# Kernel optimization log

Measured on AMD Instinct MI355X. Metric: run time of the kernel, lower is better.

Reference implementation:

```python
import jax, jax.numpy as jnp
import numpy as np

DIM = 768
HEADS = 12
DIM_HEAD = 64
INNER = HEADS * DIM_HEAD  # 768
B, N = 8, 1024
SCALE = DIM_HEAD ** -0.5


def setup_inputs() -> dict:
    key = jax.random.key(0)
    ks = jax.random.split(key, 8)
    std = 0.02
    x = jax.random.normal(ks[0], (B, N, DIM), dtype=jnp.float32)
    W_q = jax.random.normal(ks[1], (DIM, INNER), dtype=jnp.float32) * std
    W_kv = jax.random.normal(ks[2], (DIM, 2 * INNER), dtype=jnp.float32) * std
    mix_pre = jax.random.normal(ks[3], (HEADS, HEADS), dtype=jnp.float32)
    mix_post = jax.random.normal(ks[4], (HEADS, HEADS), dtype=jnp.float32)
    W_out = jax.random.normal(ks[5], (INNER, DIM), dtype=jnp.float32) * std
    b_out = jnp.zeros((DIM,), dtype=jnp.float32)
    return {"x": x, "W_q": W_q, "W_kv": W_kv, "mix_pre": mix_pre,
            "mix_post": mix_post, "W_out": W_out, "b_out": b_out}


def reference(x, W_q, W_kv, mix_pre, mix_post, W_out, b_out):
    b, n, _ = x.shape
    # projections (context == x since no cross-attn context given)
    q = x @ W_q                                   # (b, n, inner)
    kv = x @ W_kv                                 # (b, n, 2*inner)
    k, v = jnp.split(kv, 2, axis=-1)
    # (b, n, h*d) -> (b, h, n, d)
    split_heads = lambda t: t.reshape(b, n, HEADS, DIM_HEAD).transpose(0, 2, 1, 3)
    q, k, v = split_heads(q), split_heads(k), split_heads(v)
    dots = jnp.einsum('bhid,bhjd->bhij', q, k) * SCALE
    dots = jnp.einsum('bhij,hg->bgij', dots, mix_pre)    # pre-softmax talking heads
    attn = jax.nn.softmax(dots, axis=-1)
    attn = jnp.einsum('bhij,hg->bgij', attn, mix_post)   # post-softmax talking heads
    out = jnp.einsum('bhij,bhjd->bhid', attn, v)         # (b, h, n, d)
    out = out.transpose(0, 2, 1, 3).reshape(b, n, INNER)
    return out @ W_out + b_out
```

## Files before the change

### kernel.cpp

```cpp
#include <hip/hip_runtime.h>
#include <hip/hip_bf16.h>

typedef __attribute__((ext_vector_type(8))) short short8_t;
typedef __attribute__((ext_vector_type(8))) unsigned short ushort8_t;
typedef __attribute__((ext_vector_type(4))) float f32x4;

#define SCALE 0.125f

__device__ __forceinline__ unsigned short f32_to_bf16_rne(float f) {
  unsigned int u = __float_as_uint(f);
  unsigned int r = 0x7FFFu + ((u >> 16) & 1u);
  return (unsigned short)((u + r) >> 16);
}

__device__ __forceinline__ int swz(int i) { return (i + (i >> 2)) & 3; }

__global__ __launch_bounds__(256) void cast_x_kernel(const float4* __restrict__ in,
                                                     ushort4* __restrict__ out, int n4) {
  int i = blockIdx.x * 256 + threadIdx.x;
  if (i < n4) {
    float4 v = in[i];
    ushort4 o;
    o.x = f32_to_bf16_rne(v.x); o.y = f32_to_bf16_rne(v.y);
    o.z = f32_to_bf16_rne(v.z); o.w = f32_to_bf16_rne(v.w);
    out[i] = o;
  }
}

__global__ __launch_bounds__(256) void transpose_cast_kernel(const float* __restrict__ in,
                                                             unsigned short* __restrict__ out,
                                                             int R, int C) {
  __shared__ float tile[32][33];
  int c0 = blockIdx.x * 32, r0 = blockIdx.y * 32;
  int tx = threadIdx.x & 31, ty = threadIdx.x >> 5;
  #pragma unroll
  for (int i = ty; i < 32; i += 8)
    tile[i][tx] = in[(long)(r0 + i) * C + c0 + tx];
  __syncthreads();
  #pragma unroll
  for (int i = ty; i < 32; i += 8)
    out[(long)(c0 + i) * R + r0 + tx] = f32_to_bf16_rne(tile[tx][i]);
}

__global__ __launch_bounds__(256) void transpose_v_kernel(const unsigned short* __restrict__ KV,
                                                          unsigned short* __restrict__ Vt) {
  __shared__ unsigned short tile[64][72];
  const int j0 = blockIdx.x * 64, h = blockIdx.y, b = blockIdx.z;
  const int tid = threadIdx.x;
  for (int c = tid; c < 512; c += 256) {
    int j = c >> 3, dp = (c & 7) * 8;
    *(ushort8_t*)&tile[j][dp] =
        *(const ushort8_t*)&KV[(long)(b * 1024 + j0 + j) * 1536 + 768 + h * 64 + dp];
  }
  __syncthreads();
  for (int c = tid; c < 512; c += 256) {
    int d = c >> 3, jp = (c & 7) * 8;
    ushort8_t v;
    #pragma unroll
    for (int t = 0; t < 8; t++) v[t] = tile[jp + t][d];
    int jg = j0 + jp;
    int jt_ = jg >> 5;
    int u = (jg >> 3) & 3;
    *(ushort8_t*)&Vt[((long)(b * 12 + h) * 64 + d) * 1024 + (jt_ << 5) + ((u ^ swz(d)) << 3)] = v;
  }
}

template <int BM, int BN, bool OUT_F32, bool BIAS, bool SUM2>
__global__ __launch_bounds__(256) void gemm_nt(const unsigned short* __restrict__ A,
                                               const unsigned short* __restrict__ A2, int lda,
                                               const unsigned short* __restrict__ B, int ldb,
                                               void* __restrict__ Cv, int ldc,
                                               const float* __restrict__ bias,
                                               int M, int N, int K) {
  constexpr int BK = 32;
  constexpr int LDT = BK + 8;
  __shared__ unsigned short As[BM][LDT];
  __shared__ unsigned short Bs[BN][LDT];
  const int m0 = blockIdx.y * BM;
  const int n0 = blockIdx.x * BN;
  const int tid = threadIdx.x;
  const int lane = tid & 63;
  const int w = tid >> 6;
  constexpr int WM = BM / 2, WN = BN / 2;
  constexpr int FM = WM / 16, FN = WN / 16;
  const int wr = w >> 1, wc = w & 1;

  f32x4 acc[FM][FN];
  #pragma unroll
  for (int a = 0; a < FM; a++)
    #pragma unroll
    for (int b2 = 0; b2 < FN; b2++) acc[a][b2] = (f32x4){0.f, 0.f, 0.f, 0.f};

  const int rl = lane & 15;
  const int kq = (lane >> 4) * 8;

  for (int k0 = 0; k0 < K; k0 += BK) {
    __syncthreads();
    for (int c = tid; c < BM * (BK / 8); c += 256) {
      int row = c >> 2, kp = (c & 3) * 8;
      ushort8_t v = *(const ushort8_t*)&A[(long)(m0 + row) * lda + k0 + kp];
      if (SUM2) {
        ushort8_t v2 = *(const ushort8_t*)&A2[(long)(m0 + row) * lda + k0 + kp];
        #pragma unroll
        for (int x = 0; x < 8; ++x)
          v[x] = f32_to_bf16_rne(__uint_as_float((unsigned)v[x] << 16) +
                                 __uint_as_float((unsigned)v2[x] << 16));
      }
      *(ushort8_t*)&As[row][kp] = v;
    }
    for (int c = tid; c < BN * (BK / 8); c += 256) {
      int row = c >> 2, kp = (c & 3) * 8;
      *(ushort8_t*)&Bs[row][kp] = *(const ushort8_t*)&B[(long)(n0 + row) * ldb + k0 + kp];
    }
    __syncthreads();
    short8_t af[FM], bfr[FN];
    #pragma unroll
    for (int fm = 0; fm < FM; fm++) af[fm] = *(const short8_t*)&As[wr * WM + fm * 16 + rl][kq];
    #pragma unroll
    for (int fn = 0; fn < FN; fn++) bfr[fn] = *(const short8_t*)&Bs[wc * WN + fn * 16 + rl][kq];
    #pragma unroll
    for (int fm = 0; fm < FM; fm++)
      #pragma unroll
      for (int fn = 0; fn < FN; fn++)
        acc[fm][fn] = __builtin_amdgcn_mfma_f32_16x16x32_bf16(af[fm], bfr[fn], acc[fm][fn], 0, 0, 0);
  }

  const int rq4 = (lane >> 4) * 4;
  #pragma unroll
  for (int fm = 0; fm < FM; fm++)
    #pragma unroll
    for (int fn = 0; fn < FN; fn++)
      #pragma unroll
      for (int j = 0; j < 4; j++) {
        int row = m0 + wr * WM + fm * 16 + rq4 + j;
        int col = n0 + wc * WN + fn * 16 + rl;
        float v = acc[fm][fn][j];
        if (BIAS) v += bias[col];
        if (OUT_F32)
          ((float*)Cv)[(long)row * ldc + col] = v;
        else
          ((unsigned short*)Cv)[(long)row * ldc + col] = f32_to_bf16_rne(v);
      }
}

__global__ __launch_bounds__(256, 2) void qk_mix_exp_kernel(
    const unsigned short* __restrict__ Qb, const unsigned short* __restrict__ KVb,
    const float* __restrict__ mix_pre,
    unsigned short* __restrict__ Eo, float* __restrict__ Lpart, int b_base) {
  __shared__ unsigned short Kbuf[24576];
  __shared__ unsigned short Qdb[8192];
  __shared__ float mpre_s[144];
  const int jt = blockIdx.x, it = blockIdx.y, z = blockIdx.z;
  const int b = b_base + z;
  const int tid = threadIdx.x, lane = tid & 63, w = tid >> 6;
  const int r15 = lane & 15, q = lane >> 4;
  if (tid < 144) mpre_s[tid] = mix_pre[tid] * SCALE;
  const int i0 = it * 64, j0 = jt * 32;

  ushort8_t kreg[12];
  #pragma unroll
  for (int u = 0; u < 12; ++u) {
    int unit = u * 256 + tid;
    int j = unit / 96, s = unit - j * 96;
    kreg[u] = *(const ushort8_t*)&KVb[(long)(b * 1024 + j0 + j) * 1536 + ((s ^ (j & 7)) << 3)];
  }
  ushort8_t qreg[2];
  #pragma unroll
  for (int u = 0; u < 2; ++u) {
    int unit = u * 256 + tid;
    int i = unit >> 3, s = unit & 7;
    qreg[u] = *(const ushort8_t*)&Qb[(long)(b * 1024 + i0 + i) * 768 + ((s ^ (i & 7)) << 3)];
  }
  #pragma unroll
  for (int u = 0; u < 12; ++u) *(ushort8_t*)&Kbuf[(u * 256 + tid) * 8] = kreg[u];
  #pragma unroll
  for (int u = 0; u < 2; ++u) *(ushort8_t*)&Qdb[(u * 256 + tid) * 8] = qreg[u];
  __syncthreads();

  float macc[12][2][4];
  #pragma unroll
  for (int g = 0; g < 12; ++g)
    #pragma unroll
    for (int nf = 0; nf < 2; ++nf)
      #pragma unroll
      for (int e = 0; e < 4; ++e) macc[g][nf][e] = 0.f;

  const int ar = w * 16 + r15, ax = ar & 7;

  for (int h = 0; h < 12; ++h) {
    if (h < 11) {
      #pragma unroll
      for (int u = 0; u < 2; ++u) {
        int unit = u * 256 + tid;
        int i = unit >> 3, s = unit & 7;
        qreg[u] = *(const ushort8_t*)&Qb[(long)(b * 1024 + i0 + i) * 768 + (h + 1) * 64 +
                                         ((s ^ (i & 7)) << 3)];
      }
    }
    const unsigned short* Qcur = &Qdb[(h & 1) * 4096];
    short8_t a0 = *(const short8_t*)&Qcur[ar * 64 + ((q ^ ax) << 3)];
    short8_t a1 = *(const short8_t*)&Qcur[ar * 64 + (((4 + q) ^ ax) << 3)];
    f32x4 h0 = {0.f, 0.f, 0.f, 0.f}, h1 = {0.f, 0.f, 0.f, 0.f};
    {
      const int br = r15, bx = br & 7;
      short8_t b0 = *(const short8_t*)&Kbuf[br * 768 + (((h * 8 + q) ^ bx) << 3)];
      short8_t b1 = *(const short8_t*)&Kbuf[br * 768 + (((h * 8 + 4 + q) ^ bx) << 3)];
      h0 = __builtin_amdgcn_mfma_f32_16x16x32_bf16(a0, b0, h0, 0, 0, 0);
      h0 = __builtin_amdgcn_mfma_f32_16x16x32_bf16(a1, b1, h0, 0, 0, 0);
    }
    {
      const int br = 16 + r15, bx = br & 7;
      short8_t b0 = *(const short8_t*)&Kbuf[br * 768 + (((h * 8 + q) ^ bx) << 3)];
      short8_t b1 = *(const short8_t*)&Kbuf[br * 768 + (((h * 8 + 4 + q) ^ bx) << 3)];
      h1 = __builtin_amdgcn_mfma_f32_16x16x32_bf16(a0, b0, h1, 0, 0, 0);
      h1 = __builtin_amdgcn_mfma_f32_16x16x32_bf16(a1, b1, h1, 0, 0, 0);
    }
    #pragma unroll
    for (int g = 0; g < 12; ++g) {
      const float wgt = mpre_s[h * 12 + g];
      #pragma unroll
      for (int e = 0; e < 4; ++e) {
        macc[g][0][e] += wgt * h0[e];
        macc[g][1][e] += wgt * h1[e];
      }
    }
    if (h < 11) {
      unsigned short* Qnxt = &Qdb[((h + 1) & 1) * 4096];
      #pragma unroll
      for (int u = 0; u < 2; ++u) *(ushort8_t*)&Qnxt[(u * 256 + tid) * 8] = qreg[u];
    }
    __syncthreads();
  }

  #pragma unroll
  for (int g = 0; g < 12; ++g)
    #pragma unroll
    for (int nf = 0; nf < 2; ++nf)
      #pragma unroll
      for (int e = 0; e < 4; ++e) macc[g][nf][e] = __expf(macc[g][nf][e]);

  float ls[12][4];
  #pragma unroll
  for (int g = 0; g < 12; ++g)
    #pragma unroll
    for (int e = 0; e < 4; ++e) ls[g][e] = macc[g][0][e] + macc[g][1][e];
  #pragma unroll
  for (int off = 1; off < 16; off <<= 1)
    #pragma unroll
    for (int g = 0; g < 12; ++g)
      #pragma unroll
      for (int e = 0; e < 4; ++e) ls[g][e] += __shfl_xor(ls[g][e], off);
  #pragma unroll
  for (int g = 0; g < 12; ++g)
    if (r15 == g) {
      #pragma unroll
      for (int e = 0; e < 4; ++e)
        Lpart[((long)(z * 32 + jt) * 12 + g) * 1024 + i0 + w * 16 + q * 4 + e] = ls[g][e];
    }

  #pragma unroll
  for (int g = 0; g < 12; ++g)
    #pragma unroll
    for (int nf = 0; nf < 2; ++nf)
      #pragma unroll
      for (int e = 0; e < 4; ++e) {
        const int r = q * 4 + e;
        const int jsl = nf * 2 + (r15 >> 3);
        Kbuf[(w * 12 + g) * 512 + r * 32 + ((jsl ^ swz(r)) << 3) + (r15 & 7)] =
            f32_to_bf16_rne(macc[g][nf][e]);
      }
  __syncthreads();
  const long cb = ((long)((z * 32 + jt) * 16 + it)) * 24576;
  #pragma unroll
  for (int u = 0; u < 12; ++u)
    *(ushort8_t*)&Eo[cb + tid * 96 + u * 8] = *(const ushort8_t*)&Kbuf[tid * 96 + u * 8];
}

__global__ __launch_bounds__(256) void lsum_kernel(const float* __restrict__ Lpart,
                                                   float* __restrict__ invl, int nb) {
  int id = blockIdx.x * 256 + threadIdx.x;
  if (id >= nb * 12288) return;
  int z = id / 12288, r = id - z * 12288;
  float s = 0.f;
  #pragma unroll 4
  for (int jt = 0; jt < 32; ++jt) s += Lpart[((long)(z * 32 + jt)) * 12288 + r];
  invl[id] = 1.f / s;
}

__global__ __launch_bounds__(256, 1) void pv2_kernel(
    const unsigned short* __restrict__ E, const unsigned short* __restrict__ Vt,
    const float* __restrict__ invl, const float* __restrict__ mix_post,
    unsigned short* __restrict__ AOp0, unsigned short* __restrict__ AOp1, int b_base) {
  __shared__ unsigned short Ebuf[6144];
  __shared__ unsigned short Vbuf[24576];
  __shared__ unsigned short Pbuf[6144];
  const int it = blockIdx.x, jh = blockIdx.y, zc = blockIdx.z;
  const int b = b_base + zc;
  const int tid = threadIdx.x, lane = tid & 63, w = tid >> 6;
  const int r15 = lane & 15, q = lane >> 4;
  const int i_loc = tid & 15, jslot = (tid >> 4) & 3;

  float W2[3][12];
  #pragma unroll
  for (int g = 0; g < 12; ++g) {
    float il = invl[(zc * 12 + g) * 1024 + it * 16 + i_loc];
    #pragma unroll
    for (int r = 0; r < 3; ++r) W2[r][g] = mix_post[g * 12 + w * 3 + r] * il;
  }

  f32x4 acc[3][4];
  #pragma unroll
  for (int gl = 0; gl < 3; ++gl)
    #pragma unroll
    for (int df = 0; df < 4; ++df) acc[gl][df] = (f32x4){0.f, 0.f, 0.f, 0.f};

  const long vbase = (long)(b * 12) * 64 * 1024;
  ushort8_t ereg[3], vreg[12];
  auto loadE = [&](int jt) {
    const long cbs = ((long)((zc * 32 + jt) * 16 + (it >> 2))) * 24576 + (it & 3) * 6144;
    #pragma unroll
    for (int u = 0; u < 3; ++u)
      ereg[u] = *(const ushort8_t*)&E[cbs + (u * 256 + tid) * 8];
  };
  auto loadV = [&](int jt) {
    #pragma unroll
    for (int u = 0; u < 12; ++u) {
      int unit = u * 256 + tid;
      vreg[u] = *(const ushort8_t*)&Vt[vbase + (long)(unit >> 2) * 1024 + jt * 32 +
                                       ((unit & 3) << 3)];
    }
  };
  const int jt0 = jh * 16;
  loadE(jt0);
  loadV(jt0);

  for (int t = 0; t < 16; ++t) {
    __syncthreads();
    #pragma unroll
    for (int u = 0; u < 3; ++u) *(ushort8_t*)&Ebuf[(u * 256 + tid) * 8] = ereg[u];
    #pragma unroll
    for (int u = 0; u < 12; ++u) *(ushort8_t*)&Vbuf[(u * 256 + tid) * 8] = vreg[u];
    __syncthreads();
    if (t < 15) { loadE(jt0 + t + 1); loadV(jt0 + t + 1); }

    float p[3][8];
    #pragma unroll
    for (int r = 0; r < 3; ++r)
      #pragma unroll
      for (int jj = 0; jj < 8; ++jj) p[r][jj] = 0.f;
    const int esl = (jslot ^ swz(i_loc)) << 3;
    #pragma unroll
    for (int g = 0; g < 12; ++g) {
      ushort8_t ev = *(const ushort8_t*)&Ebuf[g * 512 + i_loc * 32 + esl];
      #pragma unroll
      for (int jj = 0; jj < 8; ++jj) {
        float ef = __uint_as_float((unsigned)ev[jj] << 16);
        #pragma unroll
        for (int r = 0; r < 3; ++r) p[r][jj] += W2[r][g] * ef;
      }
    }
    #pragma unroll
    for (int r = 0; r < 3; ++r) {
      ushort8_t pv;
      #pragma unroll
      for (int jj = 0; jj < 8; ++jj) pv[jj] = f32_to_bf16_rne(p[r][jj]);
      *(ushort8_t*)&Pbuf[(w * 3 + r) * 512 + i_loc * 32 + esl] = pv;
    }
    __syncthreads();

    #pragma unroll
    for (int gl = 0; gl < 3; ++gl) {
      const int g2 = w * 3 + gl;
      short8_t af = *(const short8_t*)&Pbuf[g2 * 512 + r15 * 32 + ((q ^ swz(r15)) << 3)];
      #pragma unroll
      for (int df = 0; df < 4; ++df) {
        short8_t bf = *(const short8_t*)&Vbuf[(g2 * 64 + df * 16 + r15) * 32 +
                                              ((q ^ swz(r15)) << 3)];
        acc[gl][df] = __builtin_amdgcn_mfma_f32_16x16x32_bf16(af, bf, acc[gl][df], 0, 0, 0);
      }
    }
  }

  unsigned short* AOp = jh ? AOp1 : AOp0;
  #pragma unroll
  for (int gl = 0; gl < 3; ++gl) {
    const int g2 = w * 3 + gl;
    #pragma unroll
    for (int df = 0; df < 4; ++df)
      #pragma unroll
      for (int e = 0; e < 4; ++e) {
        int row = it * 16 + q * 4 + e;
        int col = g2 * 64 + df * 16 + r15;
        AOp[(long)(b * 1024 + row) * 768 + col] = f32_to_bf16_rne(acc[gl][df][e]);
      }
  }
}

extern "C" void kernel_launch(void* const* d_in, const int* in_sizes, int n_in,
                              void* d_out, int out_size, void* d_ws, size_t ws_size,
                              hipStream_t stream) {
  const float* x        = (const float*)d_in[0];
  const float* W_q      = (const float*)d_in[1];
  const float* W_kv     = (const float*)d_in[2];
  const float* mix_pre  = (const float*)d_in[3];
  const float* mix_post = (const float*)d_in[4];
  const float* W_out    = (const float*)d_in[5];
  const float* b_out    = (const float*)d_in[6];
  float* out = (float*)d_out;

  char* p = (char*)d_ws;
  auto alloc = [&](size_t bytes) { char* r = p; p += (bytes + 255) & ~(size_t)255; return r; };
  unsigned short* xb    = (unsigned short*)alloc(8192ull * 768 * 2);
  unsigned short* WqT   = (unsigned short*)alloc(768ull * 768 * 2);
  unsigned short* WkvT  = (unsigned short*)alloc(1536ull * 768 * 2);
  unsigned short* WoutT = (unsigned short*)alloc(768ull * 768 * 2);
  unsigned short* Qb    = (unsigned short*)alloc(8192ull * 768 * 2);
  unsigned short* KVb   = (unsigned short*)alloc(8192ull * 1536 * 2);
  unsigned short* Vt    = (unsigned short*)alloc(8ull * 12 * 64 * 1024 * 2);
  unsigned short* AOp0  = (unsigned short*)alloc(8192ull * 768 * 2);
  unsigned short* AOp1  = (unsigned short*)alloc(8192ull * 768 * 2);

  const int nz = (ws_size >= 322000000ull) ? 8 : (ws_size >= 211000000ull) ? 4 : 2;
  unsigned short* E     = (unsigned short*)alloc((size_t)nz * 32 * 16 * 24576 * 2);
  float*          Lpart = (float*)alloc((size_t)nz * 32 * 12 * 1024 * 4);
  float*          invl  = (float*)alloc((size_t)nz * 12 * 1024 * 4);

  cast_x_kernel<<<6144, 256, 0, stream>>>((const float4*)x, (ushort4*)xb, 8192 * 768 / 4);
  transpose_cast_kernel<<<dim3(24, 24), 256, 0, stream>>>(W_q, WqT, 768, 768);
  transpose_cast_kernel<<<dim3(48, 24), 256, 0, stream>>>(W_kv, WkvT, 768, 1536);
  transpose_cast_kernel<<<dim3(24, 24), 256, 0, stream>>>(W_out, WoutT, 768, 768);

  gemm_nt<128, 128, false, false, false><<<dim3(6, 64), 256, 0, stream>>>(
      xb, nullptr, 768, WqT, 768, Qb, 768, nullptr, 8192, 768, 768);
  gemm_nt<128, 128, false, false, false><<<dim3(12, 64), 256, 0, stream>>>(
      xb, nullptr, 768, WkvT, 768, KVb, 1536, nullptr, 8192, 1536, 768);

  transpose_v_kernel<<<dim3(16, 12, 8), 256, 0, stream>>>(KVb, Vt);

  for (int b0 = 0; b0 < 8; b0 += nz) {
    qk_mix_exp_kernel<<<dim3(32, 16, nz), 256, 0, stream>>>(Qb, KVb, mix_pre, E, Lpart, b0);
    lsum_kernel<<<nz * 48, 256, 0, stream>>>(Lpart, invl, nz);
    pv2_kernel<<<dim3(64, 2, nz), 256, 0, stream>>>(E, Vt, invl, mix_post, AOp0, AOp1, b0);
  }

  gemm_nt<128, 128, true, true, true><<<dim3(6, 64), 256, 0, stream>>>(
      AOp0, AOp1, 768, WoutT, 768, out, 768, b_out, 8192, 768, 768);
}
```

Measured before the change: 447.9 us.

## Load Q/K MFMA fragments directly from global memory, dropping LDS staging

The QK-mix-exp kernel no longer stages K and double-buffered Q tiles in shared memory. Each lane now loads its MFMA operand fragments straight from global (or L2) memory every head iteration, which removes the per-head __syncthreads and frees LDS so the launch bound can rise to 3 blocks per CU. The pv2 kernel's launch bound is also raised to 2 blocks per CU. The trade-off is more redundant, less coalesced global loads without software prefetch, and tighter register budgets that could cause spills.

```diff
diff --git a/kernel.cpp b/kernel.cpp
--- a/kernel.cpp
+++ b/kernel.cpp
@@ -143,39 +143,23 @@
       }
 }
 
-__global__ __launch_bounds__(256, 2) void qk_mix_exp_kernel(
+__global__ __launch_bounds__(256, 3) void qk_mix_exp_kernel(
     const unsigned short* __restrict__ Qb, const unsigned short* __restrict__ KVb,
     const float* __restrict__ mix_pre,
     unsigned short* __restrict__ Eo, float* __restrict__ Lpart, int b_base) {
-  __shared__ unsigned short Kbuf[24576];
-  __shared__ unsigned short Qdb[8192];
+  __shared__ unsigned short Ebuf[24576];
   __shared__ float mpre_s[144];
   const int jt = blockIdx.x, it = blockIdx.y, z = blockIdx.z;
   const int b = b_base + z;
   const int tid = threadIdx.x, lane = tid & 63, w = tid >> 6;
   const int r15 = lane & 15, q = lane >> 4;
   if (tid < 144) mpre_s[tid] = mix_pre[tid] * SCALE;
+  __syncthreads();
   const int i0 = it * 64, j0 = jt * 32;
 
-  ushort8_t kreg[12];
-  #pragma unroll
-  for (int u = 0; u < 12; ++u) {
-    int unit = u * 256 + tid;
-    int j = unit / 96, s = unit - j * 96;
-    kreg[u] = *(const ushort8_t*)&KVb[(long)(b * 1024 + j0 + j) * 1536 + ((s ^ (j & 7)) << 3)];
-  }
-  ushort8_t qreg[2];
-  #pragma unroll
-  for (int u = 0; u < 2; ++u) {
-    int unit = u * 256 + tid;
-    int i = unit >> 3, s = unit & 7;
-    qreg[u] = *(const ushort8_t*)&Qb[(long)(b * 1024 + i0 + i) * 768 + ((s ^ (i & 7)) << 3)];
-  }
-  #pragma unroll
-  for (int u = 0; u < 12; ++u) *(ushort8_t*)&Kbuf[(u * 256 + tid) * 8] = kreg[u];
-  #pragma unroll
-  for (int u = 0; u < 2; ++u) *(ushort8_t*)&Qdb[(u * 256 + tid) * 8] = qreg[u];
-  __syncthreads();
+  const long qrow  = (long)(b * 1024 + i0 + w * 16 + r15) * 768 + q * 8;
+  const long krow0 = (long)(b * 1024 + j0 + r15) * 1536 + q * 8;
+  const long krow1 = (long)(b * 1024 + j0 + 16 + r15) * 1536 + q * 8;
 
   float macc[12][2][4];
   #pragma unroll
@@ -185,36 +169,20 @@
       #pragma unroll
       for (int e = 0; e < 4; ++e) macc[g][nf][e] = 0.f;
 
-  const int ar = w * 16 + r15, ax = ar & 7;
-
+  #pragma unroll 2
   for (int h = 0; h < 12; ++h) {
-    if (h < 11) {
-      #pragma unroll
-      for (int u = 0; u < 2; ++u) {
-        int unit = u * 256 + tid;
-        int i = unit >> 3, s = unit & 7;
-        qreg[u] = *(const ushort8_t*)&Qb[(long)(b * 1024 + i0 + i) * 768 + (h + 1) * 64 +
-                                         ((s ^ (i & 7)) << 3)];
-      }
-    }
-    const unsigned short* Qcur = &Qdb[(h & 1) * 4096];
-    short8_t a0 = *(const short8_t*)&Qcur[ar * 64 + ((q ^ ax) << 3)];
-    short8_t a1 = *(const short8_t*)&Qcur[ar * 64 + (((4 + q) ^ ax) << 3)];
+    const int kb = h * 64;
+    short8_t a0  = *(const short8_t*)&Qb[qrow + kb];
+    short8_t a1  = *(const short8_t*)&Qb[qrow + kb + 32];
+    short8_t b00 = *(const short8_t*)&KVb[krow0 + kb];
+    short8_t b01 = *(const short8_t*)&KVb[krow0 + kb + 32];
+    short8_t b10 = *(const short8_t*)&KVb[krow1 + kb];
+    short8_t b11 = *(const short8_t*)&KVb[krow1 + kb + 32];
     f32x4 h0 = {0.f, 0.f, 0.f, 0.f}, h1 = {0.f, 0.f, 0.f, 0.f};
-    {
-      const int br = r15, bx = br & 7;
-      short8_t b0 = *(const short8_t*)&Kbuf[br * 768 + (((h * 8 + q) ^ bx) << 3)];
-      short8_t b1 = *(const short8_t*)&Kbuf[br * 768 + (((h * 8 + 4 + q) ^ bx) << 3)];
-      h0 = __builtin_amdgcn_mfma_f32_16x16x32_bf16(a0, b0, h0, 0, 0, 0);
-      h0 = __builtin_amdgcn_mfma_f32_16x16x32_bf16(a1, b1, h0, 0, 0, 0);
-    }
-    {
-      const int br = 16 + r15, bx = br & 7;
-      short8_t b0 = *(const short8_t*)&Kbuf[br * 768 + (((h * 8 + q) ^ bx) << 3)];
-      short8_t b1 = *(const short8_t*)&Kbuf[br * 768 + (((h * 8 + 4 + q) ^ bx) << 3)];
-      h1 = __builtin_amdgcn_mfma_f32_16x16x32_bf16(a0, b0, h1, 0, 0, 0);
-      h1 = __builtin_amdgcn_mfma_f32_16x16x32_bf16(a1, b1, h1, 0, 0, 0);
-    }
+    h0 = __builtin_amdgcn_mfma_f32_16x16x32_bf16(a0, b00, h0, 0, 0, 0);
+    h0 = __builtin_amdgcn_mfma_f32_16x16x32_bf16(a1, b01, h0, 0, 0, 0);
+    h1 = __builtin_amdgcn_mfma_f32_16x16x32_bf16(a0, b10, h1, 0, 0, 0);
+    h1 = __builtin_amdgcn_mfma_f32_16x16x32_bf16(a1, b11, h1, 0, 0, 0);
     #pragma unroll
     for (int g = 0; g < 12; ++g) {
       const float wgt = mpre_s[h * 12 + g];
@@ -224,12 +192,6 @@
         macc[g][1][e] += wgt * h1[e];
       }
     }
-    if (h < 11) {
-      unsigned short* Qnxt = &Qdb[((h + 1) & 1) * 4096];
-      #pragma unroll
-      for (int u = 0; u < 2; ++u) *(ushort8_t*)&Qnxt[(u * 256 + tid) * 8] = qreg[u];
-    }
-    __syncthreads();
   }
 
   #pragma unroll
@@ -266,14 +228,14 @@
       for (int e = 0; e < 4; ++e) {
         const int r = q * 4 + e;
         const int jsl = nf * 2 + (r15 >> 3);
-        Kbuf[(w * 12 + g) * 512 + r * 32 + ((jsl ^ swz(r)) << 3) + (r15 & 7)] =
+        Ebuf[(w * 12 + g) * 512 + r * 32 + ((jsl ^ swz(r)) << 3) + (r15 & 7)] =
             f32_to_bf16_rne(macc[g][nf][e]);
       }
   __syncthreads();
   const long cb = ((long)((z * 32 + jt) * 16 + it)) * 24576;
   #pragma unroll
   for (int u = 0; u < 12; ++u)
-    *(ushort8_t*)&Eo[cb + tid * 96 + u * 8] = *(const ushort8_t*)&Kbuf[tid * 96 + u * 8];
+    *(ushort8_t*)&Eo[cb + (u * 256 + tid) * 8] = *(const ushort8_t*)&Ebuf[(u * 256 + tid) * 8];
 }
 
 __global__ __launch_bounds__(256) void lsum_kernel(const float* __restrict__ Lpart,
@@ -287,7 +249,7 @@
   invl[id] = 1.f / s;
 }
 
-__global__ __launch_bounds__(256, 1) void pv2_kernel(
+__global__ __launch_bounds__(256, 2) void pv2_kernel(
     const unsigned short* __restrict__ E, const unsigned short* __restrict__ Vt,
     const float* __restrict__ invl, const float* __restrict__ mix_post,
     unsigned short* __restrict__ AOp0, unsigned short* __restrict__ AOp1, int b_base) {
```

Result: slower. 636.2 us (+42.0%).
